# Performance work log

Hardware: AMD Instinct MI355X
Metric: run time of the kernel (lower is better)

## Reference

```python
import jax, jax.numpy as jnp
import numpy as np
from jax import lax

NQ = 12   # num_qubits
NL = 6    # num_layers
NC = 64   # num_classes
BATCH = 512
TWO_PI = 6.283185307179586


def _bcast(v):
    # broadcast a per-batch scalar (B,) against state (B, 2,...,2)
    return v.reshape((-1,) + (1,) * NQ) if v.ndim == 1 else v


def _apply_rx(state, theta, wire):
    """Apply RX(theta) on `wire`. state: (B,)+(2,)*NQ complex64.
    RX(t) = [[cos(t/2), -i sin(t/2)], [-i sin(t/2), cos(t/2)]]."""
    c = _bcast(jnp.cos(theta / 2))
    s = _bcast(jnp.sin(theta / 2))
    ax = 1 + wire  # wire 0 is the most significant qubit (PennyLane ordering)
    s0 = lax.index_in_dim(state, 0, ax, keepdims=True)
    s1 = lax.index_in_dim(state, 1, ax, keepdims=True)
    n0 = c * s0 - 1j * s * s1
    n1 = -1j * s * s0 + c * s1
    return jnp.concatenate([n0, n1], axis=ax)


def _apply_cnot(state, ctrl, tgt):
    ac, at = 1 + ctrl, 1 + tgt
    s0 = lax.index_in_dim(state, 0, ac, keepdims=True)
    s1 = lax.index_in_dim(state, 1, ac, keepdims=True)
    s1 = jnp.flip(s1, axis=at)  # X on target where control = 1
    return jnp.concatenate([s0, s1], axis=ac)


def _circuit(x, qweights):
    """AngleEmbedding (RX) + BasicEntanglerLayers (RX + ring CNOTs) -> <Z_i>."""
    B = x.shape[0]
    state = jnp.zeros((B,) + (2,) * NQ, jnp.complex64)
    state = state.at[(slice(None),) + (0,) * NQ].set(1.0)  # |0...0>
    # AngleEmbedding: RX(x[:, w]) on wire w (per-sample angles)
    for w in range(NQ):
        state = _apply_rx(state, x[:, w], w)
    # BasicEntanglerLayers: per layer RX rotations then ring of CNOTs
    for l in range(NL):
        for w in range(NQ):
            state = _apply_rx(state, qweights[l, w], w)
        for w in range(NQ):
            state = _apply_cnot(state, w, (w + 1) % NQ)
    probs = jnp.real(state) ** 2 + jnp.imag(state) ** 2  # (B, 2,...,2) float32
    zs = []
    for w in range(NQ):
        other = tuple(a for a in range(1, NQ + 1) if a != 1 + w)
        marg = probs.sum(axis=other)  # (B, 2)
        zs.append(marg[:, 0] - marg[:, 1])  # <Z_w>
    return jnp.stack(zs, axis=1)  # (B, NQ)


def setup_inputs() -> dict:
    key = jax.random.key(0)
    k1, k2, k3 = jax.random.split(key, 3)
    x = jax.random.normal(k1, (BATCH, NQ), dtype=jnp.float32)
    qweights = jax.random.uniform(k2, (NL, NQ), dtype=jnp.float32) * TWO_PI
    W = jax.random.normal(k3, (NC, NQ), dtype=jnp.float32) * 0.1
    b = jnp.zeros((NC,), dtype=jnp.float32)
    return {"x": x, "qweights": qweights, "W": W, "b": b}


def reference(x, qweights, W, b):
    z = _circuit(x, qweights)          # (B, NQ) expectation values
    return z @ W.T + b                  # (B, NC) classifier logits
```

## Files before the change

### kernel.cpp

```cpp
#include <hip/hip_runtime.h>

#define NQB   12
#define NST   4096
#define NLAY  6
#define NCLS  64
#define NGQ   72
#define TPB   512
#define RS    10
#define ZST   516

struct PhiArgs  { int m[NGQ]; };
struct MainArgs {
    int emlo[NQB];
    int ehi[NQB];
};

__global__ __launch_bounds__(64) void phiq_kernel(
    const float* __restrict__ qw, float* __restrict__ phiq, PhiArgs A)
{
    const int k = blockIdx.x * 64 + threadIdx.x;
    float acc = 0.f;
    #pragma unroll
    for (int g = 0; g < NGQ; ++g) {
        float v = 0.5f * qw[g];
        acc += (__popc(k & A.m[g]) & 1) ? -v : v;
    }
    phiq[k] = acc;
}

__global__ __launch_bounds__(TPB) void qnn_kernel(
    const float* __restrict__ x, const float* __restrict__ phiq,
    const float* __restrict__ W, const float* __restrict__ bias,
    float* __restrict__ out, MainArgs A)
{
    __shared__ float2 dd[TPB * RS];
    __shared__ float  zmat[NQB * ZST];
    __shared__ float  part2[NQB * 32];
    __shared__ float  zfin[NQB];

    const int tid = threadIdx.x;
    const int b   = blockIdx.x;

    float pq[8];
    #pragma unroll
    for (int r = 0; r < 8; ++r) pq[r] = phiq[tid + (r << 9)];

    float px[8];
    #pragma unroll
    for (int r = 0; r < 8; ++r) px[r] = 0.f;
    #pragma unroll
    for (int w = 0; w < NQB; ++w) {
        float xv = 0.5f * x[b * NQB + w];
        float sv = (__popc(tid & A.emlo[w]) & 1) ? -xv : xv;
        const int hi = A.ehi[w];
        #pragma unroll
        for (int r = 0; r < 8; ++r)
            px[r] += (__popc(r & hi) & 1) ? -sv : sv;
    }

    float2 myd[8];
    #pragma unroll
    for (int r = 0; r < 8; ++r) {
        float phi = pq[r] + px[r];
        float rv = phi * 0.15915494309189535f;
        rv -= floorf(rv);
        myd[r] = make_float2(__builtin_amdgcn_cosf(rv),
                             __builtin_amdgcn_sinf(rv));
    }
    {
        float4* wr = (float4*)&dd[tid * RS];
        #pragma unroll
        for (int h = 0; h < 4; ++h)
            wr[h] = make_float4(myd[2 * h].x, myd[2 * h].y,
                                myd[2 * h + 1].x, myd[2 * h + 1].y);
    }
    __syncthreads();

    float acc[NQB];
    #pragma unroll
    for (int p = 0; p < 9; ++p) {
        float aw = 0.f;
        if (!((tid >> p) & 1)) {
            const float4* row = (const float4*)&dd[(tid ^ (1 << p)) * RS];
            #pragma unroll
            for (int h = 0; h < 4; ++h) {
                float4 q = row[h];
                aw = fmaf(myd[2 * h].x, q.x, fmaf(myd[2 * h].y, q.y, aw));
                aw = fmaf(myd[2 * h + 1].x, q.z,
                          fmaf(myd[2 * h + 1].y, q.w, aw));
            }
        }
        acc[p] = aw;
    }
    {
        auto dot2 = [&](int i, int j) {
            return fmaf(myd[i].x, myd[j].x, myd[i].y * myd[j].y);
        };
        acc[9]  = dot2(0,1) + dot2(2,3) + dot2(4,5) + dot2(6,7);
        acc[10] = dot2(0,2) + dot2(1,3) + dot2(4,6) + dot2(5,7);
        acc[11] = dot2(0,4) + dot2(1,5) + dot2(2,6) + dot2(3,7);
    }

    #pragma unroll
    for (int w = 0; w < NQB; ++w) zmat[w * ZST + tid] = acc[w];
    __syncthreads();
    if (tid < NQB * 32) {
        const int w = tid >> 5, seg = tid & 31;
        const float4* rowz = (const float4*)&zmat[w * ZST];
        float s = 0.f;
        #pragma unroll
        for (int i = 0; i < 4; ++i) {
            float4 q = rowz[seg * 4 + i];
            s += (q.x + q.y) + (q.z + q.w);
        }
        part2[w * 32 + seg] = s;
    }
    __syncthreads();
    if (tid < NQB) {
        float s = 0.f;
        #pragma unroll
        for (int i = 0; i < 32; ++i) s += part2[tid * 32 + i];
        zfin[tid] = s * (2.0f / NST);
    }
    __syncthreads();

    if (tid < NCLS) {
        float a = bias[tid];
        #pragma unroll
        for (int w = 0; w < NQB; ++w) a += zfin[w] * W[tid * NQB + w];
        out[b * NCLS + tid] = a;
    }
}


static int f_of(int j) {
    for (int w = 11; w >= 0; --w) {
        int pc = 11 - w;
        int pt = 11 - ((w + 1) % 12);
        j ^= ((j >> pc) & 1) << pt;
    }
    return j;
}

static void build_args(PhiArgs* P, MainArgs* M) {
    int lm[NGQ];
    for (int l = 0; l < NLAY; ++l)
        for (int w = 0; w < NQB; ++w) {
            int v = 1 << (11 - w);
            for (int t = 0; t < l; ++t) v = f_of(v);
            lm[l * NQB + w] = v;
        }
    int col[NQB];
    for (int k = 0; k < NQB; ++k) {
        int v = 1 << k;
        for (int t = 0; t < NLAY; ++t) v = f_of(v);
        col[k] = v;
    }
    unsigned rowG[NQB], rowH[NQB];
    for (int r = 0; r < NQB; ++r) {
        unsigned rr = 0;
        for (int k = 0; k < NQB; ++k) rr |= ((unsigned)((col[k] >> r) & 1)) << k;
        rowG[r] = rr;
        rowH[r] = 1u << r;
    }
    for (int k = 0; k < NQB; ++k) {
        int piv = -1;
        for (int r = k; r < NQB; ++r)
            if ((rowG[r] >> k) & 1) { piv = r; break; }
        unsigned tg = rowG[piv], th = rowH[piv];
        rowG[piv] = rowG[k]; rowH[piv] = rowH[k];
        rowG[k] = tg; rowH[k] = th;
        for (int r = 0; r < NQB; ++r)
            if (r != k && ((rowG[r] >> k) & 1)) { rowG[r] ^= rowG[k]; rowH[r] ^= rowH[k]; }
    }
    int meas_nat[NQB];
    for (int w = 0; w < NQB; ++w) meas_nat[w] = (int)rowH[11 - w];

    int Tm[NQB];
    for (int w = 0; w < NQB; ++w) Tm[w] = meas_nat[w];
    auto xf = [&](int m) {
        int o = 0;
        for (int bb = 0; bb < NQB; ++bb)
            if (__builtin_popcount((unsigned)(Tm[bb] & m)) & 1) o |= 1 << bb;
        return o;
    };
    for (int g = 0; g < NGQ; ++g) P->m[g] = xf(lm[g]);
    for (int w = 0; w < NQB; ++w) {
        int e = xf(1 << (11 - w));
        M->emlo[w] = e & 511;
        M->ehi[w]  = e >> 9;
    }
}

extern "C" void kernel_launch(void* const* d_in, const int* in_sizes, int n_in,
                              void* d_out, int out_size, void* d_ws, size_t ws_size,
                              hipStream_t stream) {
    const float* x    = (const float*)d_in[0];
    const float* qw   = (const float*)d_in[1];
    const float* W    = (const float*)d_in[2];
    const float* bias = (const float*)d_in[3];
    float* out        = (float*)d_out;
    float* phiq       = (float*)d_ws;

    PhiArgs P; MainArgs M;
    build_args(&P, &M);

    const int batch = in_sizes[0] / NQB;
    phiq_kernel<<<64, 64, 0, stream>>>(qw, phiq, P);
    qnn_kernel<<<batch, TPB, 0, stream>>>(x, phiq, W, bias, out, M);
}
```

Before: 66.79 us.

## Fuse phase precompute into main kernel with constexpr masks and butterfly

Removes the separate phiq kernel and the global phase buffer. Each thread now builds its eight phases from 84 signed terms, binned by the high mask bits and combined with a 3-stage butterfly. The gate masks become constexpr, so the host-side mask building and kernel-argument passing also go away. The cost is more per-thread ALU work in every block, traded for one fewer kernel launch and no dependent global read.

New measurement: 63.63 us. 4.7% less time.

```diff
diff --git a/kernel.cpp b/kernel.cpp
--- a/kernel.cpp
+++ b/kernel.cpp
@@ -1,4 +1,5 @@
 #include <hip/hip_runtime.h>
+#include <utility>
 
 #define NQB   12
 #define NST   4096
@@ -9,29 +10,87 @@
 #define RS    10
 #define ZST   516
 
-struct PhiArgs  { int m[NGQ]; };
-struct MainArgs {
-    int emlo[NQB];
-    int ehi[NQB];
-};
-
-__global__ __launch_bounds__(64) void phiq_kernel(
-    const float* __restrict__ qw, float* __restrict__ phiq, PhiArgs A)
-{
-    const int k = blockIdx.x * 64 + threadIdx.x;
-    float acc = 0.f;
-    #pragma unroll
+
+struct Masks { int m[NGQ]; int em[NQB]; };
+
+constexpr int pc_c(unsigned v) { int c = 0; while (v) { c += (int)(v & 1u); v >>= 1; } return c; }
+
+constexpr int f_of_c(int j) {
+    for (int w = 11; w >= 0; --w) {
+        int pc = 11 - w;
+        int pt = 11 - ((w + 1) % 12);
+        j ^= ((j >> pc) & 1) << pt;
+    }
+    return j;
+}
+
+constexpr Masks build_masks() {
+    Masks M{};
+    int lm[NGQ] = {};
+    for (int l = 0; l < NLAY; ++l)
+        for (int w = 0; w < NQB; ++w) {
+            int v = 1 << (11 - w);
+            for (int t = 0; t < l; ++t) v = f_of_c(v);
+            lm[l * NQB + w] = v;
+        }
+    int col[NQB] = {};
+    for (int k = 0; k < NQB; ++k) {
+        int v = 1 << k;
+        for (int t = 0; t < NLAY; ++t) v = f_of_c(v);
+        col[k] = v;
+    }
+    unsigned rowG[NQB] = {}, rowH[NQB] = {};
+    for (int r = 0; r < NQB; ++r) {
+        unsigned rr = 0;
+        for (int k = 0; k < NQB; ++k) rr |= ((unsigned)((col[k] >> r) & 1)) << k;
+        rowG[r] = rr;
+        rowH[r] = 1u << r;
+    }
+    for (int k = 0; k < NQB; ++k) {
+        int piv = -1;
+        for (int r = k; r < NQB; ++r)
+            if ((rowG[r] >> k) & 1) { piv = r; break; }
+        unsigned tg = rowG[piv], th = rowH[piv];
+        rowG[piv] = rowG[k]; rowH[piv] = rowH[k];
+        rowG[k] = tg; rowH[k] = th;
+        for (int r = 0; r < NQB; ++r)
+            if (r != k && ((rowG[r] >> k) & 1)) { rowG[r] ^= rowG[k]; rowH[r] ^= rowH[k]; }
+    }
+    int meas_nat[NQB] = {};
+    for (int w = 0; w < NQB; ++w) meas_nat[w] = (int)rowH[11 - w];
+
+    int Tm[NQB] = {};
+    for (int w = 0; w < NQB; ++w) Tm[w] = meas_nat[w];
     for (int g = 0; g < NGQ; ++g) {
-        float v = 0.5f * qw[g];
-        acc += (__popc(k & A.m[g]) & 1) ? -v : v;
-    }
-    phiq[k] = acc;
+        int mm = lm[g], o = 0;
+        for (int bb = 0; bb < NQB; ++bb)
+            if (pc_c((unsigned)(Tm[bb] & mm)) & 1) o |= 1 << bb;
+        M.m[g] = o;
+    }
+    for (int w = 0; w < NQB; ++w) {
+        int mm = 1 << (11 - w), o = 0;
+        for (int bb = 0; bb < NQB; ++bb)
+            if (pc_c((unsigned)(Tm[bb] & mm)) & 1) o |= 1 << bb;
+        M.em[w] = o;
+    }
+    return M;
+}
+
+constexpr Masks MK = build_masks();
+
+template <typename F, int... Is>
+__device__ __forceinline__ void static_for_impl(F f, std::integer_sequence<int, Is...>) {
+    (f(std::integral_constant<int, Is>{}), ...);
+}
+template <int N, typename F>
+__device__ __forceinline__ void static_for(F f) {
+    static_for_impl(f, std::make_integer_sequence<int, N>{});
 }
 
 __global__ __launch_bounds__(TPB) void qnn_kernel(
-    const float* __restrict__ x, const float* __restrict__ phiq,
+    const float* __restrict__ x, const float* __restrict__ qw,
     const float* __restrict__ W, const float* __restrict__ bias,
-    float* __restrict__ out, MainArgs A)
+    float* __restrict__ out)
 {
     __shared__ float2 dd[TPB * RS];
     __shared__ float  zmat[NQB * ZST];
@@ -41,27 +100,37 @@
     const int tid = threadIdx.x;
     const int b   = blockIdx.x;
 
-    float pq[8];
-    #pragma unroll
-    for (int r = 0; r < 8; ++r) pq[r] = phiq[tid + (r << 9)];
-
-    float px[8];
-    #pragma unroll
-    for (int r = 0; r < 8; ++r) px[r] = 0.f;
-    #pragma unroll
-    for (int w = 0; w < NQB; ++w) {
-        float xv = 0.5f * x[b * NQB + w];
-        float sv = (__popc(tid & A.emlo[w]) & 1) ? -xv : xv;
-        const int hi = A.ehi[w];
-        #pragma unroll
-        for (int r = 0; r < 8; ++r)
-            px[r] += (__popc(r & hi) & 1) ? -sv : sv;
-    }
+    float C[8];
+    #pragma unroll
+    for (int h = 0; h < 8; ++h) C[h] = 0.f;
+
+    static_for<NGQ>([&](auto gc) {
+        constexpr int g  = decltype(gc)::value;
+        constexpr int mg = MK.m[g];
+        constexpr int lo = mg & 511;
+        constexpr int hi = mg >> 9;
+        float v = 0.5f * qw[g];
+        C[hi] += (__popc(tid & lo) & 1) ? -v : v;
+    });
+    static_for<NQB>([&](auto wc) {
+        constexpr int w  = decltype(wc)::value;
+        constexpr int mg = MK.em[w];
+        constexpr int lo = mg & 511;
+        constexpr int hi = mg >> 9;
+        float v = 0.5f * x[b * NQB + w];
+        C[hi] += (__popc(tid & lo) & 1) ? -v : v;
+    });
+
+    #define BFLY(i, j) { float a_ = C[i], b_ = C[j]; C[i] = a_ + b_; C[j] = a_ - b_; }
+    BFLY(0,1) BFLY(2,3) BFLY(4,5) BFLY(6,7)
+    BFLY(0,2) BFLY(1,3) BFLY(4,6) BFLY(5,7)
+    BFLY(0,4) BFLY(1,5) BFLY(2,6) BFLY(3,7)
+    #undef BFLY
 
     float2 myd[8];
     #pragma unroll
     for (int r = 0; r < 8; ++r) {
-        float phi = pq[r] + px[r];
+        float phi = C[r];
         float rv = phi * 0.15915494309189535f;
         rv -= floorf(rv);
         myd[r] = make_float2(__builtin_amdgcn_cosf(rv),
@@ -132,66 +201,6 @@
     }
 }
 
-
-static int f_of(int j) {
-    for (int w = 11; w >= 0; --w) {
-        int pc = 11 - w;
-        int pt = 11 - ((w + 1) % 12);
-        j ^= ((j >> pc) & 1) << pt;
-    }
-    return j;
-}
-
-static void build_args(PhiArgs* P, MainArgs* M) {
-    int lm[NGQ];
-    for (int l = 0; l < NLAY; ++l)
-        for (int w = 0; w < NQB; ++w) {
-            int v = 1 << (11 - w);
-            for (int t = 0; t < l; ++t) v = f_of(v);
-            lm[l * NQB + w] = v;
-        }
-    int col[NQB];
-    for (int k = 0; k < NQB; ++k) {
-        int v = 1 << k;
-        for (int t = 0; t < NLAY; ++t) v = f_of(v);
-        col[k] = v;
-    }
-    unsigned rowG[NQB], rowH[NQB];
-    for (int r = 0; r < NQB; ++r) {
-        unsigned rr = 0;
-        for (int k = 0; k < NQB; ++k) rr |= ((unsigned)((col[k] >> r) & 1)) << k;
-        rowG[r] = rr;
-        rowH[r] = 1u << r;
-    }
-    for (int k = 0; k < NQB; ++k) {
-        int piv = -1;
-        for (int r = k; r < NQB; ++r)
-            if ((rowG[r] >> k) & 1) { piv = r; break; }
-        unsigned tg = rowG[piv], th = rowH[piv];
-        rowG[piv] = rowG[k]; rowH[piv] = rowH[k];
-        rowG[k] = tg; rowH[k] = th;
-        for (int r = 0; r < NQB; ++r)
-            if (r != k && ((rowG[r] >> k) & 1)) { rowG[r] ^= rowG[k]; rowH[r] ^= rowH[k]; }
-    }
-    int meas_nat[NQB];
-    for (int w = 0; w < NQB; ++w) meas_nat[w] = (int)rowH[11 - w];
-
-    int Tm[NQB];
-    for (int w = 0; w < NQB; ++w) Tm[w] = meas_nat[w];
-    auto xf = [&](int m) {
-        int o = 0;
-        for (int bb = 0; bb < NQB; ++bb)
-            if (__builtin_popcount((unsigned)(Tm[bb] & m)) & 1) o |= 1 << bb;
-        return o;
-    };
-    for (int g = 0; g < NGQ; ++g) P->m[g] = xf(lm[g]);
-    for (int w = 0; w < NQB; ++w) {
-        int e = xf(1 << (11 - w));
-        M->emlo[w] = e & 511;
-        M->ehi[w]  = e >> 9;
-    }
-}
-
 extern "C" void kernel_launch(void* const* d_in, const int* in_sizes, int n_in,
                               void* d_out, int out_size, void* d_ws, size_t ws_size,
                               hipStream_t stream) {
@@ -200,12 +209,8 @@
     const float* W    = (const float*)d_in[2];
     const float* bias = (const float*)d_in[3];
     float* out        = (float*)d_out;
-    float* phiq       = (float*)d_ws;
-
-    PhiArgs P; MainArgs M;
-    build_args(&P, &M);
+    (void)d_ws; (void)ws_size;
 
     const int batch = in_sizes[0] / NQB;
-    phiq_kernel<<<64, 64, 0, stream>>>(qw, phiq, P);
-    qnn_kernel<<<batch, TPB, 0, stream>>>(x, phiq, W, bias, out, M);
-}
+    qnn_kernel<<<batch, TPB, 0, stream>>>(x, qw, W, bias, out);
+}
```
